# Kernel tuning notes

Hardware: AMD Instinct MI355X
Metric: run time of the kernel (lower is better)

Reference implementation:

```python
import jax, jax.numpy as jnp
import numpy as np

# -------- configuration (production-scale segmentation head) --------
BS, C, H, W = 8, 256, 96, 96
N = H * W          # nodes in the spanning tree (flattened pixels)
E = N - 1          # spanning-tree edge count
ZETA_G = 0.01      # default zeta_g of Global_APro.forward


def setup_inputs() -> dict:
    key = jax.random.key(0)
    k1, k2 = jax.random.split(key)
    feature_in = jax.random.normal(k1, (BS, 1, H, W), dtype=jnp.float32)
    # scaled so norm2 distances over C=256 channels stay O(1..10)
    embed_in = 0.1 * jax.random.normal(k2, (BS, C, H, W), dtype=jnp.float32)
    # Random spanning trees, one per batch element. Edges are topologically
    # ordered: edge e connects parent=src[e] < child=tgt[e]=e+1, so processing
    # edges in order is a valid root->leaf sweep (and reversed is leaf->root).
    rng = np.random.default_rng(0)
    trees = []
    children = np.arange(1, N, dtype=np.int32)
    for _ in range(BS):
        parents = np.floor(rng.random(E) * np.arange(1, N)).astype(np.int32)
        trees.append(np.stack([parents, children], axis=1))
    tree = jnp.asarray(np.stack(trees, axis=0))  # [BS, E, 2] int32
    return {"feature_in": feature_in, "embed_in": embed_in, "tree": tree}


def _gp_single(f, wgt, src, tgt):
    """Global affinity propagation (tree filter) on one tree.
    Computes out_i = sum_j A_ij f_j / sum_j A_ij with A_ij = prod of edge
    affinities along the unique tree path i->j, via the classic two-pass DP.
    f: [N], wgt/src/tgt: [E] (edges topologically ordered, parent=src).
    """
    ones = jnp.ones_like(f)

    def up(carry, xs):                 # leaf -> root aggregation
        S, Z = carry
        s, t, we = xs
        S = S.at[s].add(we * S[t])
        Z = Z.at[s].add(we * Z[t])
        return (S, Z), None

    (S, Z), _ = jax.lax.scan(up, (f, ones), (src, tgt, wgt), reverse=True)

    def down(carry, xs):               # root -> leaf propagation
        F, G = carry
        s, t, we = xs
        F = F.at[t].set(we * F[s] + (1.0 - we * we) * F[t])
        G = G.at[t].set(we * G[s] + (1.0 - we * we) * G[t])
        return (F, G), None

    (F, G), _ = jax.lax.scan(down, (S, Z), (src, tgt, wgt))
    return F / G


def reference(feature_in, embed_in, tree):
    bs, c, h, w = embed_in.shape
    n = h * w
    emb = embed_in.reshape(bs, c, n)               # [bs, c, N]
    src = tree[:, :, 0]                            # [bs, E]
    tgt = tree[:, :, 1]                            # [bs, E]
    # gather node embeddings along tree edges (get_true_index)
    gather = jax.vmap(lambda e, i: e[:, i])        # [c, N], [E] -> [c, E]
    src_node = gather(emb, src)                    # [bs, c, E]
    tgt_node = gather(emb, tgt)                    # [bs, c, E]
    diff = src_node - tgt_node
    dist = jnp.sum(diff * diff, axis=1)            # norm2_distance -> [bs, E]
    wgt = jnp.exp(-ZETA_G * dist)                  # edge affinity
    f = feature_in.reshape(bs, n)                  # [bs, N]
    out = jax.vmap(_gp_single)(f, wgt, src, tgt)   # [bs, N]
    return out.reshape(bs, 1, h, w)
```

## Files before the change

### kernel.cpp

```cpp
#include <hip/hip_runtime.h>
#include <hip/hip_bf16.h>
#include <hip/hip_fp16.h>

#define BS 8
#define C  256
#define N  9216
#define E  9215
#define MAXD 128
#define LVL_STRIDE 192
#define TSLABS (N / 64)
#define NARROW 64

__global__ __launch_bounds__(1024) void setup_kernel(const float* __restrict__ emb,
                                                     __half* __restrict__ embT,
                                                     const int* __restrict__ tree,
                                                     int2* __restrict__ tswG,
                                                     int* __restrict__ slotG,
                                                     int* __restrict__ lvlOff) {
    __shared__ int P[N];
    __shared__ int U[N];
    __shared__ int SLOT[N];
    __shared__ int cnt8[MAXD * 8];
    __shared__ int tot[MAXD];
    __shared__ int sc1[MAXD];
    __shared__ int off[MAXD + 1];
    __shared__ int maxd_sh;
    const int tid = threadIdx.x;

    if (blockIdx.x >= BS) {
        const int tb = blockIdx.x - BS;
        const int b  = tb & 7;
        const int n0 = (tb >> 3) * 64;
        __half (*tile)[65] = (__half(*)[65])P;

        const int nn = tid & 63;
        const int cg = tid >> 6;
        const float* src = emb + (size_t)b * C * N + n0;
        #pragma unroll
        for (int k = 0; k < 16; ++k) {
            int cc = cg * 16 + k;
            tile[cc][nn] = __float2half(src[(size_t)cc * N + nn]);
        }
        __syncthreads();

        const int cp = tid & 127;
        const int ng = tid >> 7;
        __half* dst = embT + ((size_t)b * N + n0) * C;
        #pragma unroll
        for (int k = 0; k < 8; ++k) {
            int n2 = ng * 8 + k;
            __half2 v = __halves2half2(tile[2 * cp][n2], tile[2 * cp + 1][n2]);
            *(__half2*)(dst + (size_t)n2 * C + 2 * cp) = v;
        }
        return;
    }

    const int b = blockIdx.x;
    const int* tb = tree + b * E * 2;

    for (int t = tid; t < N; t += 1024)
        P[t] = (t == 0) ? 0 : (tb[(t - 1) * 2] | (1 << 16));
    for (int i = tid; i < MAXD * 8; i += 1024) cnt8[i] = 0;
    if (tid == 0) maxd_sh = 1;
    __syncthreads();

    for (int r = 0; r < 3; ++r) {
        for (int t = tid; t < N; t += 1024) {
            int p = P[t];
            int a = p & 0xffff;
            if (a == 0) U[t] = p;
            else {
                int pa = P[a];
                U[t] = (pa & 0xffff) | (((p >> 16) + (pa >> 16)) << 16);
            }
        }
        __syncthreads();
        for (int t = tid; t < N; t += 1024) {
            int p = U[t];
            int a = p & 0xffff;
            if (a == 0) P[t] = p;
            else {
                int pa = U[a];
                P[t] = (pa & 0xffff) | (((p >> 16) + (pa >> 16)) << 16);
            }
        }
        __syncthreads();
    }

    for (int t = 1 + tid; t < N; t += 1024) {
        int d = P[t] >> 16;
        atomicAdd(&cnt8[d * 8 + (tid >> 7)], 1);
    }
    __syncthreads();

    for (int d = tid; d < MAXD; d += 1024) {
        int s = 0;
        #pragma unroll
        for (int k = 0; k < 8; ++k) {
            int v = cnt8[d * 8 + k];
            cnt8[d * 8 + k] = s;
            s += v;
        }
        tot[d] = s;
        if (s > 0) atomicMax(&maxd_sh, d);
    }
    __syncthreads();

    {
        int* src = tot; int* dst = sc1;
        for (int step = 1; step < MAXD; step <<= 1) {
            for (int d = tid; d < MAXD; d += 1024)
                dst[d] = src[d] + ((d >= step) ? src[d - step] : 0);
            __syncthreads();
            int* tmp = src; src = dst; dst = tmp;
        }
        for (int d = tid; d < MAXD; d += 1024) off[d + 1] = src[d];
        if (tid == 0) off[0] = 0;
    }
    __syncthreads();

    if (tid == 0) {
        int md = maxd_sh;
        int lo = 0;
        while (lo < md && off[lo + 2] - off[lo + 1] <= NARROW) ++lo;
        int hi = md + 1;
        while (hi > lo + 1 && off[hi] - off[hi - 1] <= NARROW) --hi;
        lvlOff[b * LVL_STRIDE + 129] = md;
        lvlOff[b * LVL_STRIDE + 130] = lo;
        lvlOff[b * LVL_STRIDE + 131] = hi;
    }
    for (int t = 1 + tid; t < N; t += 1024) {
        int d = P[t] >> 16;
        int idx = atomicAdd(&cnt8[d * 8 + (tid >> 7)], 1);
        int slot = off[d] + idx;
        int p = tb[(t - 1) * 2];
        U[slot] = t | (p << 16);
        SLOT[t - 1] = slot;
    }
    __syncthreads();

    for (int i = tid; i < E; i += 1024) {
        tswG[b * N + i] = make_int2(U[i], 0);
        slotG[b * N + i] = SLOT[i];
    }
    for (int i = tid; i <= MAXD; i += 1024) lvlOff[b * LVL_STRIDE + i] = off[i];
}

__global__ __launch_bounds__(256) void weights_kernel(const __half* __restrict__ embT,
                                                      const int* __restrict__ tree,
                                                      const int* __restrict__ slotG,
                                                      int2* __restrict__ tswG) {
    const int b   = blockIdx.y;
    const int tid = threadIdx.x;
    const int lane = tid & 63;
    const int wid  = tid >> 6;
    const int sub  = lane >> 5;
    const int l    = lane & 31;
    const int e    = (blockIdx.x * 4 + wid) * 2 + sub;

    float acc = 0.f;
    if (e < E) {
        int s = tree[(b * E + e) * 2];
        int t = e + 1;
        const float4* ps = (const float4*)(embT + ((size_t)b * N + s) * C) + l;
        const float4* pt = (const float4*)(embT + ((size_t)b * N + t) * C) + l;
        float4 av = *ps;
        float4 bv = *pt;
        const __half2* ah = (const __half2*)&av;
        const __half2* bh = (const __half2*)&bv;
        #pragma unroll
        for (int j = 0; j < 4; ++j) {
            float2 fa = __half22float2(ah[j]);
            float2 fb = __half22float2(bh[j]);
            float d0 = fa.x - fb.x;
            float d1 = fa.y - fb.y;
            acc += d0 * d0 + d1 * d1;
        }
    }
    #pragma unroll
    for (int m = 16; m >= 1; m >>= 1) acc += __shfl_xor(acc, m);
    if (l == 0 && e < E) {
        int slot = slotG[b * N + e];
        tswG[b * N + slot].y = __float_as_int(__expf(-0.01f * acc));
    }
}

__device__ __forceinline__ void up_edge(float2* V, const int2& ew) {
    int t = ew.x & 0xffff, p = ew.x >> 16;
    float w = __int_as_float(ew.y);
    float2 vt = V[t];
    atomicAdd(&V[p].x, w * vt.x);
    atomicAdd(&V[p].y, w * vt.y);
}

__device__ __forceinline__ void down_edge(float2* V, const int2& ew) {
    int t = ew.x & 0xffff, s = ew.x >> 16;
    float w = __int_as_float(ew.y);
    float2 vs = V[s], vt = V[t];
    float c = 1.f - w * w;
    V[t] = make_float2(w * vs.x + c * vt.x, w * vs.y + c * vt.y);
}

__global__ __launch_bounds__(512) void dp_kernel(const float* __restrict__ feat,
                                                 const int* __restrict__ lvlOff,
                                                 const int2* __restrict__ tswG,
                                                 float* __restrict__ out) {
    const int b = blockIdx.x;
    const int tid = threadIdx.x;
    __shared__ float2 V[N];
    __shared__ int2 TSW[N];
    __shared__ int off[MAXD + 1];
    __shared__ int meta[3];

    for (int i = tid; i <= MAXD; i += 512) off[i] = lvlOff[b * LVL_STRIDE + i];
    if (tid < 3) meta[tid] = lvlOff[b * LVL_STRIDE + 129 + tid];

    const int2* tG = tswG + b * N;
    for (int i = tid; i < N; i += 512)
        V[i] = make_float2(feat[b * N + i], 1.0f);
    for (int i = tid; i < E; i += 512)
        TSW[i] = tG[i];
    __syncthreads();
    const int maxd = meta[0], loE = meta[1], hiS = meta[2];

    if (tid < 64) {
        for (int lev = maxd; lev >= hiS; --lev) {
            int s0 = off[lev], s1 = off[lev + 1];
            for (int i = s0 + tid; i < s1; i += 64) up_edge(V, TSW[i]);
            __threadfence_block();
        }
    }
    __syncthreads();
    for (int lev = hiS - 1; lev > loE; --lev) {
        int s0 = off[lev], s1 = off[lev + 1];
        for (int i = s0 + tid; i < s1; i += 512) up_edge(V, TSW[i]);
        __syncthreads();
    }
    if (tid < 64) {
        for (int lev = loE; lev >= 1; --lev) {
            int s0 = off[lev], s1 = off[lev + 1];
            for (int i = s0 + tid; i < s1; i += 64) up_edge(V, TSW[i]);
            __threadfence_block();
        }
    }
    __syncthreads();

    if (tid < 64) {
        for (int lev = 1; lev <= loE; ++lev) {
            int s0 = off[lev], s1 = off[lev + 1];
            for (int i = s0 + tid; i < s1; i += 64) down_edge(V, TSW[i]);
            __threadfence_block();
        }
    }
    __syncthreads();
    for (int lev = loE + 1; lev < hiS; ++lev) {
        int s0 = off[lev], s1 = off[lev + 1];
        for (int i = s0 + tid; i < s1; i += 512) down_edge(V, TSW[i]);
        __syncthreads();
    }
    if (tid < 64) {
        for (int lev = hiS; lev <= maxd; ++lev) {
            int s0 = off[lev], s1 = off[lev + 1];
            for (int i = s0 + tid; i < s1; i += 64) down_edge(V, TSW[i]);
            __threadfence_block();
        }
    }
    __syncthreads();

    for (int i = tid; i < N; i += 512) {
        float2 v = V[i];
        out[b * N + i] = v.x / v.y;
    }
}

extern "C" void kernel_launch(void* const* d_in, const int* in_sizes, int n_in,
                              void* d_out, int out_size, void* d_ws, size_t ws_size,
                              hipStream_t stream) {
    const float* feat = (const float*)d_in[0];
    const float* emb  = (const float*)d_in[1];
    const int*   tree = (const int*)d_in[2];
    float* out = (float*)d_out;

    const size_t BN = (size_t)BS * N;
    int2* tswG   = (int2*)d_ws;
    int*  slotG  = (int*)((char*)d_ws + BN * 8);
    int*  lvlOff = (int*)((char*)d_ws + BN * 12);
    __half* embT = (__half*)((char*)d_ws +
                    ((BN * 12 + BS * LVL_STRIDE * 4 + 255) / 256) * 256);

    setup_kernel<<<BS + TSLABS * BS, 1024, 0, stream>>>(emb, embT, tree, tswG, slotG, lvlOff);
    weights_kernel<<<dim3((E + 7) / 8, BS), 256, 0, stream>>>(embT, tree, slotG, tswG);
    dp_kernel<<<BS, 512, 0, stream>>>(feat, lvlOff, tswG, out);
}
```

Before: 171.3 us.

## Compute edge distances channel-sliced in setup kernel, drop transpose and weights kernel

Replaces the fp16 transpose of the embeddings and the separate per-edge weights kernel with channel-group blocks. Each block loads 4 full channel rows into shared memory, accumulates squared differences for all edges, and atomically adds them into a global distance array. The exp and slot mapping move into the dp kernel's load phase, which removes one launch, the transposed half-precision copy and the slot indirection. In exchange it adds a memset, many float atomics (non-deterministic summation order) and full fp32 reads of the embeddings.

After: 170.8 us. No clear change (-0.3%).

```diff
diff --git a/kernel.cpp b/kernel.cpp
--- a/kernel.cpp
+++ b/kernel.cpp
@@ -8,18 +8,17 @@
 #define E  9215
 #define MAXD 128
 #define LVL_STRIDE 192
-#define TSLABS (N / 64)
 #define NARROW 64
+#define CPG 4
+#define NG  (C / CPG)
 
 __global__ __launch_bounds__(1024) void setup_kernel(const float* __restrict__ emb,
-                                                     __half* __restrict__ embT,
                                                      const int* __restrict__ tree,
-                                                     int2* __restrict__ tswG,
-                                                     int* __restrict__ slotG,
+                                                     float* __restrict__ distG,
+                                                     int* __restrict__ uparr,
                                                      int* __restrict__ lvlOff) {
     __shared__ int P[N];
     __shared__ int U[N];
-    __shared__ int SLOT[N];
     __shared__ int cnt8[MAXD * 8];
     __shared__ int tot[MAXD];
     __shared__ int sc1[MAXD];
@@ -28,29 +27,40 @@
     const int tid = threadIdx.x;
 
     if (blockIdx.x >= BS) {
-        const int tb = blockIdx.x - BS;
-        const int b  = tb & 7;
-        const int n0 = (tb >> 3) * 64;
-        __half (*tile)[65] = (__half(*)[65])P;
-
-        const int nn = tid & 63;
-        const int cg = tid >> 6;
-        const float* src = emb + (size_t)b * C * N + n0;
-        #pragma unroll
-        for (int k = 0; k < 16; ++k) {
-            int cc = cg * 16 + k;
-            tile[cc][nn] = __float2half(src[(size_t)cc * N + nn]);
-        }
-        __syncthreads();
-
-        const int cp = tid & 127;
-        const int ng = tid >> 7;
-        __half* dst = embT + ((size_t)b * N + n0) * C;
-        #pragma unroll
-        for (int k = 0; k < 8; ++k) {
-            int n2 = ng * 8 + k;
-            __half2 v = __halves2half2(tile[2 * cp][n2], tile[2 * cp + 1][n2]);
-            *(__half2*)(dst + (size_t)n2 * C + 2 * cp) = v;
+        const int wb = blockIdx.x - BS;
+        const int b  = wb & 7;
+        const int c0 = (wb >> 3) * CPG;
+        float* row = (float*)P;
+
+        int se[9];
+        #pragma unroll
+        for (int k = 0; k < 9; ++k) {
+            int e = tid + k * 1024;
+            se[k] = (e < E) ? tree[((size_t)b * E + e) * 2] : 0;
+        }
+        float acc[9];
+        #pragma unroll
+        for (int k = 0; k < 9; ++k) acc[k] = 0.f;
+
+        for (int cc = 0; cc < CPG; ++cc) {
+            const float4* rp = (const float4*)(emb + ((size_t)b * C + c0 + cc) * N);
+            for (int j = tid; j < N / 4; j += 1024)
+                ((float4*)row)[j] = rp[j];
+            __syncthreads();
+            #pragma unroll
+            for (int k = 0; k < 9; ++k) {
+                int e = tid + k * 1024;
+                if (e < E) {
+                    float d = row[se[k]] - row[e + 1];
+                    acc[k] += d * d;
+                }
+            }
+            __syncthreads();
+        }
+        #pragma unroll
+        for (int k = 0; k < 9; ++k) {
+            int e = tid + k * 1024;
+            if (e < E) atomicAdd(&distG[(size_t)b * N + e], acc[k]);
         }
         return;
     }
@@ -135,54 +145,11 @@
         int slot = off[d] + idx;
         int p = tb[(t - 1) * 2];
         U[slot] = t | (p << 16);
-        SLOT[t - 1] = slot;
-    }
-    __syncthreads();
-
-    for (int i = tid; i < E; i += 1024) {
-        tswG[b * N + i] = make_int2(U[i], 0);
-        slotG[b * N + i] = SLOT[i];
-    }
+    }
+    __syncthreads();
+
+    for (int i = tid; i < E; i += 1024) uparr[b * N + i] = U[i];
     for (int i = tid; i <= MAXD; i += 1024) lvlOff[b * LVL_STRIDE + i] = off[i];
-}
-
-__global__ __launch_bounds__(256) void weights_kernel(const __half* __restrict__ embT,
-                                                      const int* __restrict__ tree,
-                                                      const int* __restrict__ slotG,
-                                                      int2* __restrict__ tswG) {
-    const int b   = blockIdx.y;
-    const int tid = threadIdx.x;
-    const int lane = tid & 63;
-    const int wid  = tid >> 6;
-    const int sub  = lane >> 5;
-    const int l    = lane & 31;
-    const int e    = (blockIdx.x * 4 + wid) * 2 + sub;
-
-    float acc = 0.f;
-    if (e < E) {
-        int s = tree[(b * E + e) * 2];
-        int t = e + 1;
-        const float4* ps = (const float4*)(embT + ((size_t)b * N + s) * C) + l;
-        const float4* pt = (const float4*)(embT + ((size_t)b * N + t) * C) + l;
-        float4 av = *ps;
-        float4 bv = *pt;
-        const __half2* ah = (const __half2*)&av;
-        const __half2* bh = (const __half2*)&bv;
-        #pragma unroll
-        for (int j = 0; j < 4; ++j) {
-            float2 fa = __half22float2(ah[j]);
-            float2 fb = __half22float2(bh[j]);
-            float d0 = fa.x - fb.x;
-            float d1 = fa.y - fb.y;
-            acc += d0 * d0 + d1 * d1;
-        }
-    }
-    #pragma unroll
-    for (int m = 16; m >= 1; m >>= 1) acc += __shfl_xor(acc, m);
-    if (l == 0 && e < E) {
-        int slot = slotG[b * N + e];
-        tswG[b * N + slot].y = __float_as_int(__expf(-0.01f * acc));
-    }
 }
 
 __device__ __forceinline__ void up_edge(float2* V, const int2& ew) {
@@ -203,7 +170,8 @@
 
 __global__ __launch_bounds__(512) void dp_kernel(const float* __restrict__ feat,
                                                  const int* __restrict__ lvlOff,
-                                                 const int2* __restrict__ tswG,
+                                                 const int* __restrict__ uparr,
+                                                 const float* __restrict__ distG,
                                                  float* __restrict__ out) {
     const int b = blockIdx.x;
     const int tid = threadIdx.x;
@@ -215,11 +183,15 @@
     for (int i = tid; i <= MAXD; i += 512) off[i] = lvlOff[b * LVL_STRIDE + i];
     if (tid < 3) meta[tid] = lvlOff[b * LVL_STRIDE + 129 + tid];
 
-    const int2* tG = tswG + b * N;
+    const int* uA = uparr + b * N;
+    const float* dG = distG + b * N;
     for (int i = tid; i < N; i += 512)
         V[i] = make_float2(feat[b * N + i], 1.0f);
-    for (int i = tid; i < E; i += 512)
-        TSW[i] = tG[i];
+    for (int i = tid; i < E; i += 512) {
+        int ts = uA[i];
+        float ds = dG[(ts & 0xffff) - 1];
+        TSW[i] = make_int2(ts, __float_as_int(__expf(-0.01f * ds)));
+    }
     __syncthreads();
     const int maxd = meta[0], loE = meta[1], hiS = meta[2];
 
@@ -282,13 +254,11 @@
     float* out = (float*)d_out;
 
     const size_t BN = (size_t)BS * N;
-    int2* tswG   = (int2*)d_ws;
-    int*  slotG  = (int*)((char*)d_ws + BN * 8);
-    int*  lvlOff = (int*)((char*)d_ws + BN * 12);
-    __half* embT = (__half*)((char*)d_ws +
-                    ((BN * 12 + BS * LVL_STRIDE * 4 + 255) / 256) * 256);
-
-    setup_kernel<<<BS + TSLABS * BS, 1024, 0, stream>>>(emb, embT, tree, tswG, slotG, lvlOff);
-    weights_kernel<<<dim3((E + 7) / 8, BS), 256, 0, stream>>>(embT, tree, slotG, tswG);
-    dp_kernel<<<BS, 512, 0, stream>>>(feat, lvlOff, tswG, out);
-}
+    float* distG  = (float*)d_ws;
+    int*   uparr  = (int*)((char*)d_ws + BN * 4);
+    int*   lvlOff = (int*)((char*)d_ws + BN * 8);
+
+    hipMemsetAsync(distG, 0, BN * sizeof(float), stream);
+    setup_kernel<<<BS + BS * NG, 1024, 0, stream>>>(emb, tree, distG, uparr, lvlOff);
+    dp_kernel<<<BS, 512, 0, stream>>>(feat, lvlOff, uparr, distG, out);
+}
```
